# Kernel tuning notes

Measured on AMD Instinct MI355X. Metric: run time of the kernel, lower is better.

The kernel has to match this reference:

```python
import jax, jax.numpy as jnp
import numpy as np

B_, L_, D_ = 4, 4096, 256
EXPAND = 2
DI_ = EXPAND * D_      # 512 inner channels
H_ = 8                 # heads
P_ = DI_ // H_         # 64 head dim
N_ = 16                # d_state
K_ = 3                 # depthwise conv kernel


def setup_inputs() -> dict:
    key = jax.random.key(0)
    ks = jax.random.split(key, 32)

    def n(i, shape, s=0.02):
        return jax.random.normal(ks[i], shape, jnp.float32) * s

    inp = {"inputs": jax.random.normal(ks[0], (B_, L_, D_), jnp.float32)}
    i = 1
    for pre in ("f_", "b_"):
        inp[pre + "in_proj_w"] = n(i, (2 * DI_, D_)); i += 1
        inp[pre + "in_proj_b"] = jnp.zeros((2 * DI_,), jnp.float32)
        inp[pre + "x_proj_w"] = n(i, (DI_ + 2 * H_ * N_, DI_)); i += 1
        inp[pre + "x_proj_b"] = jnp.zeros((DI_ + 2 * H_ * N_,), jnp.float32)
        inp[pre + "dt_bias"] = jnp.full((DI_,), -4.0, jnp.float32)  # softplus -> small dt
        inp[pre + "A_log"] = jnp.log(jnp.tile(jnp.arange(1, N_ + 1, dtype=jnp.float32), (DI_, 1)))
        inp[pre + "D_skip"] = jnp.ones((DI_,), jnp.float32)
        inp[pre + "out_proj_w"] = n(i, (D_, DI_)); i += 1
        inp[pre + "out_proj_b"] = jnp.zeros((D_,), jnp.float32)
    inp["norm_w"] = jnp.ones((D_,), jnp.float32)
    inp["norm_b"] = jnp.zeros((D_,), jnp.float32)
    inp["conv_w"] = n(20, (D_, 1, K_), 0.1)   # depthwise: (out_ch, in_ch/groups=1, k)
    inp["conv_b"] = jnp.zeros((D_,), jnp.float32)
    return inp


def _layernorm(x, w, b):
    m = x.mean(-1, keepdims=True)
    v = ((x - m) ** 2).mean(-1, keepdims=True)
    return (x - m) * jax.lax.rsqrt(v + 1e-5) * w + b


def _mh_ssm(x, in_w, in_b, xp_w, xp_b, dt_b, A_log, D_skip, out_w, out_b):
    # Multihead selective-scan SSM (Mamba-style). x: (B, L, D)
    Bsz, L, _ = x.shape
    xz = x @ in_w.T + in_b                      # (B, L, 2*DI)
    xi, z = jnp.split(xz, 2, axis=-1)
    xi = jax.nn.silu(xi)                        # (B, L, DI)
    proj = xi @ xp_w.T + xp_b                   # (B, L, DI + 2*H*N)
    dt = jax.nn.softplus(proj[..., :DI_] + dt_b)        # (B, L, DI)
    Bm = proj[..., DI_:DI_ + H_ * N_].reshape(Bsz, L, H_, N_)
    Cm = proj[..., DI_ + H_ * N_:].reshape(Bsz, L, H_, N_)
    A = -jnp.exp(A_log).reshape(H_, P_, N_)     # (H, P, N), negative
    x4 = xi.reshape(Bsz, L, H_, P_)
    dt4 = dt.reshape(Bsz, L, H_, P_)

    def step(h, t):
        xt, dtt, Bt, Ct = t                     # (B,H,P), (B,H,P), (B,H,N), (B,H,N)
        dA = jnp.exp(dtt[..., None] * A)        # (B,H,P,N)
        h = h * dA + dtt[..., None] * Bt[:, :, None, :] * xt[..., None]
        y = jnp.einsum('bhpn,bhn->bhp', h, Ct)
        return h, y

    xs = (x4.transpose(1, 0, 2, 3), dt4.transpose(1, 0, 2, 3),
          Bm.transpose(1, 0, 2, 3), Cm.transpose(1, 0, 2, 3))
    h0 = jnp.zeros((Bsz, H_, P_, N_), x.dtype)
    _, ys = jax.lax.scan(step, h0, xs)          # ys: (L,B,H,P)
    y = ys.transpose(1, 0, 2, 3).reshape(Bsz, L, DI_) + xi * D_skip
    y = y * jax.nn.silu(z)                      # gating
    return y @ out_w.T + out_b                  # (B, L, D)


def reference(inputs,
              f_in_proj_w, f_in_proj_b, f_x_proj_w, f_x_proj_b, f_dt_bias,
              f_A_log, f_D_skip, f_out_proj_w, f_out_proj_b,
              b_in_proj_w, b_in_proj_b, b_x_proj_w, b_x_proj_b, b_dt_bias,
              b_A_log, b_D_skip, b_out_proj_w, b_out_proj_b,
              norm_w, norm_b, conv_w, conv_b):
    # Cascaded bidirectional SSM: backward(flip(norm(forward(x)))) then flip back
    y1 = _mh_ssm(inputs, f_in_proj_w, f_in_proj_b, f_x_proj_w, f_x_proj_b,
                 f_dt_bias, f_A_log, f_D_skip, f_out_proj_w, f_out_proj_b)
    y1n = jnp.flip(_layernorm(y1, norm_w, norm_b), axis=1)
    y2 = _mh_ssm(y1n, b_in_proj_w, b_in_proj_b, b_x_proj_w, b_x_proj_b,
                 b_dt_bias, b_A_log, b_D_skip, b_out_proj_w, b_out_proj_b)
    out = jnp.flip(y2, axis=1)
    # locality branch: depthwise Conv1d (groups=C) + exact GELU
    xt = inputs.transpose(0, 2, 1)              # (B, C, L)
    c = jax.lax.conv_general_dilated(
        xt, conv_w, window_strides=(1,), padding=[(1, 1)],
        dimension_numbers=('NCH', 'OIH', 'NCH'), feature_group_count=D_)
    c = jax.nn.gelu(c + conv_b[None, :, None], approximate=False)
    return out + c.transpose(0, 2, 1)
```

## Files before the change

### kernel.cpp

```cpp
#include <hip/hip_runtime.h>
#include <hip/hip_bf16.h>
#include <cstdint>
#include <cstddef>

#define B_  4
#define L_  4096
#define D_  256
#define DI_ 512
#define H_  8
#define P_  64
#define N_  16
#define M_  (B_ * L_)
#define PROJ_ (DI_ + 2 * H_ * N_)

#define NC_ 64
#define CL_ (L_ / NC_)
#define NSEQ_ (B_ * H_ * P_ * N_)
#define LOG2E_ 1.4426950408889634f

typedef __bf16 bf16x8 __attribute__((ext_vector_type(8)));
typedef __bf16 bf16x4 __attribute__((ext_vector_type(4)));
typedef float f32x4 __attribute__((ext_vector_type(4)));
typedef _Float16 f16x8 __attribute__((ext_vector_type(8)));

__device__ __forceinline__ void cp16_lds(const __hip_bfloat16* g, short* lds) {
    __builtin_amdgcn_global_load_lds(
        (const __attribute__((address_space(1))) void*)g,
        (__attribute__((address_space(3))) void*)lds, 16, 0, 0);
}

#define WS1 (2 * DI_ * D_)
#define WS2 (PROJ_ * DI_)
#define WS3 (D_ * DI_)
#define WC1 (WS1)
#define WC2 (WC1 + WS2)
#define WC3 (WC2 + WS3)
#define WC4 (WC3 + WS1)
#define WC5 (WC4 + WS2)
#define WC6 (WC5 + WS3)
#define WT8 (WC6 / 8)

__launch_bounds__(256)
__global__ void f2b_all(const float* __restrict__ i1,
                        const float* __restrict__ i2, const float* __restrict__ i3,
                        const float* __restrict__ i4, const float* __restrict__ i5,
                        const float* __restrict__ i6,
                        __hip_bfloat16* o1, __hip_bfloat16* o2,
                        __hip_bfloat16* o3, __hip_bfloat16* o4, __hip_bfloat16* o5,
                        __hip_bfloat16* o6) {
    for (int idx8 = blockIdx.x * 256 + threadIdx.x; idx8 < WT8;
         idx8 += gridDim.x * 256) {
        const int idx = idx8 * 8;
        const float* s; __hip_bfloat16* d; int off;
        if (idx < WC1)      { s = i1; d = o1; off = idx; }
        else if (idx < WC2) { s = i2; d = o2; off = idx - WC1; }
        else if (idx < WC3) { s = i3; d = o3; off = idx - WC2; }
        else if (idx < WC4) { s = i4; d = o4; off = idx - WC3; }
        else if (idx < WC5) { s = i5; d = o5; off = idx - WC4; }
        else                { s = i6; d = o6; off = idx - WC5; }
        const float4 f0 = *reinterpret_cast<const float4*>(s + off);
        const float4 f1 = *reinterpret_cast<const float4*>(s + off + 4);
        bf16x8 v;
        v[0] = (__bf16)f0.x; v[1] = (__bf16)f0.y;
        v[2] = (__bf16)f0.z; v[3] = (__bf16)f0.w;
        v[4] = (__bf16)f1.x; v[5] = (__bf16)f1.y;
        v[6] = (__bf16)f1.z; v[7] = (__bf16)f1.w;
        *reinterpret_cast<bf16x8*>(d + off) = v;
    }
}

template <int EPI, int AF32>
__launch_bounds__(256)
__global__ void gemm_mfma(const __hip_bfloat16* __restrict__ A,
                          const __hip_bfloat16* __restrict__ W,
                          const float* __restrict__ bias, int Kv,
                          __hip_bfloat16* __restrict__ zb,
                          __hip_bfloat16* __restrict__ obf,
                          const float* __restrict__ aux,
                          const float* __restrict__ A32) {
    __shared__ short As[128 * 64];
    __shared__ short Bs[128 * 64];
    const int tid = threadIdx.x;
    const int lane = tid & 63;
    const int wave = tid >> 6;
    const int bm = blockIdx.x * 128;
    const int bn = blockIdx.y * 128;
    const int wm = (wave >> 1) * 64;
    const int wn = (wave & 1) * 64;

    f32x4 acc[4][4];
#pragma unroll
    for (int i = 0; i < 4; ++i)
#pragma unroll
        for (int j = 0; j < 4; ++j) acc[i][j] = (f32x4)0.f;

    const int srow = lane >> 3;
    const int sx = lane & 7;
    const int ssegx = (sx ^ srow) * 8;
    const __hip_bfloat16* gA0 = A + (size_t)(bm + wave * 32 + srow) * Kv + ssegx;
    const __hip_bfloat16* gB0 = W + (size_t)(bn + wave * 32 + srow) * Kv + ssegx;
    short* lA0 = As + (wave * 32) * 64;
    short* lB0 = Bs + (wave * 32) * 64;

    const int fr = lane & 15;
    const int kq = lane >> 4;

    for (int k0 = 0; k0 < Kv; k0 += 64) {
        if (AF32) {
#pragma unroll
            for (int rb = 0; rb < 4; ++rb) {
                const int row = wave * 32 + rb * 8 + srow;
                const float* g = A32 + (size_t)(bm + row) * Kv + k0 + ssegx;
                const float4 f0 = *reinterpret_cast<const float4*>(g);
                const float4 f1 = *reinterpret_cast<const float4*>(g + 4);
                bf16x8 s;
                s[0] = (__bf16)f0.x; s[1] = (__bf16)f0.y;
                s[2] = (__bf16)f0.z; s[3] = (__bf16)f0.w;
                s[4] = (__bf16)f1.x; s[5] = (__bf16)f1.y;
                s[6] = (__bf16)f1.z; s[7] = (__bf16)f1.w;
                *reinterpret_cast<bf16x8*>(&As[row * 64 + sx * 8]) = s;
            }
        } else {
#pragma unroll
            for (int rb = 0; rb < 4; ++rb)
                cp16_lds(gA0 + (size_t)(rb * 8) * Kv + k0, lA0 + rb * 8 * 64);
        }
#pragma unroll
        for (int rb = 0; rb < 4; ++rb)
            cp16_lds(gB0 + (size_t)(rb * 8) * Kv + k0, lB0 + rb * 8 * 64);
        __syncthreads();
#pragma unroll
        for (int ks = 0; ks < 2; ++ks) {
            const int kgg = ks * 4 + kq;
            const int kslot = (kgg ^ (fr & 7)) * 8;
            bf16x8 af[4], bv[4];
#pragma unroll
            for (int i = 0; i < 4; ++i)
                af[i] = *reinterpret_cast<const bf16x8*>(
                    &As[(wm + i * 16 + fr) * 64 + kslot]);
#pragma unroll
            for (int j = 0; j < 4; ++j)
                bv[j] = *reinterpret_cast<const bf16x8*>(
                    &Bs[(wn + j * 16 + fr) * 64 + kslot]);
#pragma unroll
            for (int i = 0; i < 4; ++i)
#pragma unroll
                for (int j = 0; j < 4; ++j)
                    acc[i][j] = __builtin_amdgcn_mfma_f32_16x16x32_bf16(
                        af[i], bv[j], acc[i][j], 0, 0, 0);
        }
        __syncthreads();
    }

    const int n16 = lane & 15;
    const int r4 = (lane >> 4) * 4;
#pragma unroll
    for (int i = 0; i < 4; ++i) {
#pragma unroll
        for (int j = 0; j < 4; ++j) {
            const int cg = bn + wn + j * 16 + n16;
            const float bb = bias[cg];
#pragma unroll
            for (int v = 0; v < 4; ++v) {
                const int r = bm + wm + i * 16 + r4 + v;
                float val = acc[i][j][v] + bb;
                if (EPI == 1) {
                    if (cg < DI_) {
                        val = val / (1.f + __expf(-val));
                        obf[(size_t)r * DI_ + cg] = __float2bfloat16(val);
                    } else {
                        zb[(size_t)r * DI_ + cg - DI_] = __float2bfloat16(val);
                    }
                } else {
                    if (cg < DI_) {
                        const float x = val + aux[cg];
                        val = (x > 20.f) ? x : __logf(1.f + __expf(x));
                    }
                    obf[(size_t)r * PROJ_ + cg] = __float2bfloat16(val);
                }
            }
        }
    }
}

__launch_bounds__(256)
__global__ void gemm64_convout(const __hip_bfloat16* __restrict__ A,
                               const __hip_bfloat16* __restrict__ W,
                               const float* __restrict__ bias, int Kv,
                               float* __restrict__ out0,
                               const float* __restrict__ cw,
                               const float* __restrict__ cb,
                               const float* __restrict__ cinp) {
    __shared__ short As[64 * 64];
    __shared__ short Bs[64 * 64];
    const int tid = threadIdx.x;
    const int lane = tid & 63;
    const int wave = tid >> 6;
    const int bm = blockIdx.x * 64;
    const int bn = blockIdx.y * 64;
    const int wm = (wave >> 1) * 32;
    const int wn = (wave & 1) * 32;

    f32x4 acc[2][2];
#pragma unroll
    for (int i = 0; i < 2; ++i)
#pragma unroll
        for (int j = 0; j < 2; ++j) acc[i][j] = (f32x4)0.f;

    const int srow = lane >> 3;
    const int ssegx = ((lane & 7) ^ srow) * 8;
    const __hip_bfloat16* gA0 = A + (size_t)(bm + wave * 16 + srow) * Kv + ssegx;
    const __hip_bfloat16* gB0 = W + (size_t)(bn + wave * 16 + srow) * Kv + ssegx;
    short* lA0 = As + (wave * 16) * 64;
    short* lB0 = Bs + (wave * 16) * 64;

    const int fr = lane & 15;
    const int kq = lane >> 4;

    for (int k0 = 0; k0 < Kv; k0 += 64) {
#pragma unroll
        for (int rb = 0; rb < 2; ++rb) {
            cp16_lds(gA0 + (size_t)(rb * 8) * Kv + k0, lA0 + rb * 8 * 64);
            cp16_lds(gB0 + (size_t)(rb * 8) * Kv + k0, lB0 + rb * 8 * 64);
        }
        __syncthreads();
#pragma unroll
        for (int ks = 0; ks < 2; ++ks) {
            const int kgg = ks * 4 + kq;
            const int kslot = (kgg ^ (fr & 7)) * 8;
            bf16x8 af[2], bv[2];
#pragma unroll
            for (int i = 0; i < 2; ++i)
                af[i] = *reinterpret_cast<const bf16x8*>(
                    &As[(wm + i * 16 + fr) * 64 + kslot]);
#pragma unroll
            for (int j = 0; j < 2; ++j)
                bv[j] = *reinterpret_cast<const bf16x8*>(
                    &Bs[(wn + j * 16 + fr) * 64 + kslot]);
#pragma unroll
            for (int i = 0; i < 2; ++i)
#pragma unroll
                for (int j = 0; j < 2; ++j)
                    acc[i][j] = __builtin_amdgcn_mfma_f32_16x16x32_bf16(
                        af[i], bv[j], acc[i][j], 0, 0, 0);
        }
        __syncthreads();
    }

    const int n16 = lane & 15;
    const int r4 = (lane >> 4) * 4;
#pragma unroll
    for (int i = 0; i < 2; ++i) {
#pragma unroll
        for (int j = 0; j < 2; ++j) {
            const int cg = bn + wn + j * 16 + n16;
            const float bb = bias[cg];
#pragma unroll
            for (int v = 0; v < 4; ++v) {
                const int r = bm + wm + i * 16 + r4 + v;
                float val = acc[i][j][v] + bb;
                const int b = r >> 12;
                const int l = r & (L_ - 1);
                const int lo = L_ - 1 - l;
                const size_t base = ((size_t)(b << 12) + lo) * 256 + cg;
                float cv = fmaf(cinp[base], cw[cg * 3 + 1], cb[cg]);
                if (lo > 0) cv = fmaf(cinp[base - 256], cw[cg * 3 + 0], cv);
                if (lo + 1 < L_) cv = fmaf(cinp[base + 256], cw[cg * 3 + 2], cv);
                const float g = 0.5f * cv * (1.f + erff(cv * 0.70710678118654752f));
                out0[base] = val + g;
            }
        }
    }
}

__launch_bounds__(256)
__global__ void gemm_out_ln(const __hip_bfloat16* __restrict__ A,
                            const __hip_bfloat16* __restrict__ W,
                            const float* __restrict__ bias,
                            const float* __restrict__ lnw,
                            const float* __restrict__ lnb,
                            __hip_bfloat16* __restrict__ outb) {
    __shared__ short As[64 * 64];
    __shared__ short Ws[256 * 64];
    __shared__ float rs[2][4][64];
    const int tid = threadIdx.x;
    const int lane = tid & 63;
    const int wave = tid >> 6;
    const int bm = blockIdx.x * 64;
    const int Kv = DI_;

    f32x4 acc[4][4];
#pragma unroll
    for (int i = 0; i < 4; ++i)
#pragma unroll
        for (int j = 0; j < 4; ++j) acc[i][j] = (f32x4)0.f;

    const int srow = lane >> 3;
    const int ssegx = ((lane & 7) ^ srow) * 8;
    const __hip_bfloat16* gA0 = A + (size_t)(bm + wave * 16 + srow) * Kv + ssegx;
    const __hip_bfloat16* gW0 = W + (size_t)(wave * 64 + srow) * Kv + ssegx;
    short* lA0 = As + (wave * 16) * 64;
    short* lW0 = Ws + (wave * 64) * 64;

    const int fr = lane & 15;
    const int kq = lane >> 4;

    for (int k0 = 0; k0 < Kv; k0 += 64) {
#pragma unroll
        for (int rb = 0; rb < 2; ++rb)
            cp16_lds(gA0 + (size_t)(rb * 8) * Kv + k0, lA0 + rb * 8 * 64);
#pragma unroll
        for (int rb = 0; rb < 8; ++rb)
            cp16_lds(gW0 + (size_t)(rb * 8) * Kv + k0, lW0 + rb * 8 * 64);
        __syncthreads();
#pragma unroll
        for (int ks = 0; ks < 2; ++ks) {
            const int kgg = ks * 4 + kq;
            const int kslot = (kgg ^ (fr & 7)) * 8;
            bf16x8 af[4], bv[4];
#pragma unroll
            for (int i = 0; i < 4; ++i)
                af[i] = *reinterpret_cast<const bf16x8*>(
                    &As[(i * 16 + fr) * 64 + kslot]);
#pragma unroll
            for (int j = 0; j < 4; ++j)
                bv[j] = *reinterpret_cast<const bf16x8*>(
                    &Ws[(wave * 64 + j * 16 + fr) * 64 + kslot]);
#pragma unroll
            for (int i = 0; i < 4; ++i)
#pragma unroll
                for (int j = 0; j < 4; ++j)
                    acc[i][j] = __builtin_amdgcn_mfma_f32_16x16x32_bf16(
                        af[i], bv[j], acc[i][j], 0, 0, 0);
        }
        __syncthreads();
    }

    const int n16 = lane & 15;
    const int r4 = (lane >> 4) * 4;
#pragma unroll
    for (int j = 0; j < 4; ++j) {
        const float bb = bias[wave * 64 + j * 16 + n16];
#pragma unroll
        for (int i = 0; i < 4; ++i)
#pragma unroll
            for (int v = 0; v < 4; ++v) acc[i][j][v] += bb;
    }

#pragma unroll
    for (int i = 0; i < 4; ++i) {
#pragma unroll
        for (int v = 0; v < 4; ++v) {
            float s = 0.f, s2 = 0.f;
#pragma unroll
            for (int j = 0; j < 4; ++j) {
                const float t = acc[i][j][v];
                s += t; s2 = fmaf(t, t, s2);
            }
            s += __shfl_xor(s, 1); s2 += __shfl_xor(s2, 1);
            s += __shfl_xor(s, 2); s2 += __shfl_xor(s2, 2);
            s += __shfl_xor(s, 4); s2 += __shfl_xor(s2, 4);
            s += __shfl_xor(s, 8); s2 += __shfl_xor(s2, 8);
            if (n16 == 0) {
                rs[0][wave][i * 16 + r4 + v] = s;
                rs[1][wave][i * 16 + r4 + v] = s2;
            }
        }
    }
    __syncthreads();

#pragma unroll
    for (int i = 0; i < 4; ++i) {
#pragma unroll
        for (int v = 0; v < 4; ++v) {
            const int row = i * 16 + r4 + v;
            const float ts = rs[0][0][row] + rs[0][1][row] + rs[0][2][row] + rs[0][3][row];
            const float ts2 = rs[1][0][row] + rs[1][1][row] + rs[1][2][row] + rs[1][3][row];
            const float mean = ts * (1.f / 256.f);
            const float var = ts2 * (1.f / 256.f) - mean * mean;
            const float inv = rsqrtf(var + 1e-5f);
            const int rg = bm + row;
            const int b = rg >> 12;
            const int l = rg & (L_ - 1);
            const size_t drow = (size_t)((b << 12) + (L_ - 1 - l)) * 256;
#pragma unroll
            for (int j = 0; j < 4; ++j) {
                const int cg = wave * 64 + j * 16 + n16;
                const float o = (acc[i][j][v] - mean) * inv * lnw[cg] + lnb[cg];
                outb[drow + cg] = __float2bfloat16(o);
            }
        }
    }
}

__device__ __forceinline__ bool a_is_arith(const float* A2) {
    bool ok = true;
#pragma unroll
    for (int n = 1; n < N_; ++n)
        ok = ok && (fabsf(A2[n] - (float)(n + 1) * A2[0]) <= 1e-4f * fabsf(A2[n]));
    return ok;
}

__launch_bounds__(256)
__global__ void scan_chunk_state(const __hip_bfloat16* __restrict__ xi,
                                 const __hip_bfloat16* __restrict__ projb,
                                 const float* __restrict__ A_log,
                                 float* __restrict__ sS,
                                 _Float16* __restrict__ st_hend) {
    __shared__ float bsh[4][CL_][16];
    const int bh = blockIdx.x;
    const int b = bh >> 3;
    const int h = bh & 7;
    const int lane = threadIdx.x & 63;
    const int wave = threadIdx.x >> 6;
    const int chunk = blockIdx.y * 4 + wave;
    const int t0 = chunk * CL_;
    const int c = h * P_ + lane;
    const int bOff = DI_ + h * N_;

    {
#pragma unroll
        for (int r = 0; r < 4; ++r) {
            const int stp = r * 16 + (lane >> 2);
            const int j = (lane & 3) * 4;
            const bf16x4 v = *reinterpret_cast<const bf16x4*>(
                projb + ((size_t)b * L_ + t0 + stp) * PROJ_ + bOff + j);
            *reinterpret_cast<float4*>(&bsh[wave][stp][j]) =
                make_float4((float)v[0], (float)v[1], (float)v[2], (float)v[3]);
        }
    }

    float A2[N_], hs[N_];
#pragma unroll
    for (int n = 0; n < N_; ++n) {
        A2[n] = -__expf(A_log[c * N_ + n]) * LOG2E_;
        hs[n] = 0.f;
    }
    const bool fast = a_is_arith(A2);

    const __hip_bfloat16* pDt = projb + ((size_t)b * L_ + t0) * PROJ_ + c;
    const __hip_bfloat16* px = xi + ((size_t)b * L_ + t0) * DI_ + c;
    float S = 0.f;

    if (fast) {
        float dtb[2][4], xb[2][4];
#pragma unroll
        for (int i = 0; i < 4; ++i) {
            dtb[0][i] = __bfloat162float(pDt[(size_t)i * PROJ_]);
            xb[0][i] = __bfloat162float(px[(size_t)i * DI_]);
        }
#pragma unroll
        for (int k = 0; k < CL_ / 4; ++k) {
            const int cur = k & 1, nxt = cur ^ 1;
            if (k + 1 < CL_ / 4) {
#pragma unroll
                for (int i = 0; i < 4; ++i) {
                    dtb[nxt][i] = __bfloat162float(pDt[(size_t)((k + 1) * 4 + i) * PROJ_]);
                    xb[nxt][i] = __bfloat162float(px[(size_t)((k + 1) * 4 + i) * DI_]);
                }
            }
#pragma unroll
            for (int i = 0; i < 4; ++i) {
                const int t = k * 4 + i;
                const float dt_v = dtb[cur][i];
                const float dtx = dt_v * xb[cur][i];
                const float e1 = exp2f(dt_v * A2[0]);
                S += dt_v;
                const f32x4* bp = reinterpret_cast<const f32x4*>(&bsh[wave][t][0]);
                float dA = e1;
#pragma unroll
                for (int q = 0; q < 4; ++q) {
                    const f32x4 Bq = bp[q];
#pragma unroll
                    for (int j = 0; j < 4; ++j) {
                        hs[q * 4 + j] = fmaf(hs[q * 4 + j], dA, dtx * Bq[j]);
                        dA *= e1;
                    }
                }
            }
        }
    } else {
#pragma unroll 4
        for (int t = 0; t < CL_; ++t) {
            const float dt_v = __bfloat162float(pDt[(size_t)t * PROJ_]);
            const float xv = __bfloat162float(px[(size_t)t * DI_]);
            const float dtx = dt_v * xv;
            S += dt_v;
#pragma unroll
            for (int n = 0; n < N_; ++n) {
                const float dA = exp2f(dt_v * A2[n]);
                hs[n] = fmaf(hs[n], dA, dtx * bsh[wave][t][n]);
            }
        }
    }

    sS[(size_t)chunk * (B_ * DI_) + (size_t)(bh * P_ + lane)] = S;
    const size_t s0 = (size_t)chunk * NSEQ_ + ((size_t)(bh * P_ + lane)) * N_;
    f16x8 h0, h1;
#pragma unroll
    for (int j = 0; j < 8; ++j) { h0[j] = (_Float16)hs[j]; h1[j] = (_Float16)hs[8 + j]; }
    *reinterpret_cast<f16x8*>(st_hend + s0) = h0;
    *reinterpret_cast<f16x8*>(st_hend + s0 + 8) = h1;
}

__launch_bounds__(128)
__global__ void scan_combine(const float* __restrict__ sS,
                             const float* __restrict__ A_log,
                             _Float16* __restrict__ st_prod,
                             const _Float16* __restrict__ st_hend) {
    const int gtid = blockIdx.x * 128 + threadIdx.x;
    const int s = gtid >> 1;
    const int u = gtid & 1;
    const int lane = threadIdx.x & 63;
    const int seqc = s >> 4;
    const int n = s & 15;
    const int cA = seqc & (DI_ - 1);
    const float A2n = -__expf(A_log[cA * N_ + n]) * LOG2E_;

    float Hloc[32], Dr[32];
    float H = 0.f, D = 1.f;
#pragma unroll
    for (int kk = 0; kk < 32; ++kk) {
        const int k = u * 32 + kk;
        const size_t o = (size_t)k * NSEQ_ + s;
        const float Pv = exp2f(A2n * sS[(size_t)k * (B_ * DI_) + seqc]);
        const float Ev = (float)st_hend[o];
        Hloc[kk] = H; Dr[kk] = D;
        H = fmaf(Pv, H, Ev);
        D *= Pv;
    }
    const float Hmid = __shfl(H, lane & ~1);
    if (u == 0) {
#pragma unroll
        for (int kk = 0; kk < 32; ++kk) {
            const size_t o = (size_t)kk * NSEQ_ + s;
            st_prod[o] = (_Float16)Hloc[kk];
        }
    } else {
#pragma unroll
        for (int kk = 0; kk < 32; ++kk) {
            const size_t o = (size_t)(32 + kk) * NSEQ_ + s;
            st_prod[o] = (_Float16)fmaf(Dr[kk], Hmid, Hloc[kk]);
        }
    }
}

__launch_bounds__(256)
__global__ void scan_chunk_out(const __hip_bfloat16* __restrict__ xi,
                               const __hip_bfloat16* __restrict__ z,
                               const __hip_bfloat16* __restrict__ projb,
                               const float* __restrict__ A_log,
                               const float* __restrict__ D_skip,
                               const _Float16* __restrict__ st_hin,
                               __hip_bfloat16* __restrict__ yg) {
    __shared__ float bc[4][CL_][32];
    const int bh = blockIdx.x;
    const int b = bh >> 3;
    const int h = bh & 7;
    const int lane = threadIdx.x & 63;
    const int wave = threadIdx.x >> 6;
    const int chunk = blockIdx.y * 4 + wave;
    const int t0 = chunk * CL_;
    const int c = h * P_ + lane;
    const int bOff = DI_ + h * N_;
    const int cOff = DI_ + H_ * N_ + h * N_;

    {
#pragma unroll
        for (int r = 0; r < 8; ++r) {
            const int stp = r * 8 + (lane >> 3);
            const int j = (lane & 7) * 4;
            const int soff = (j < 16) ? (bOff + j) : (cOff + (j - 16));
            const bf16x4 v = *reinterpret_cast<const bf16x4*>(
                projb + ((size_t)b * L_ + t0 + stp) * PROJ_ + soff);
            *reinterpret_cast<float4*>(&bc[wave][stp][j]) =
                make_float4((float)v[0], (float)v[1], (float)v[2], (float)v[3]);
        }
    }

    float A2[N_], hs[N_];
    const size_t s0 = (size_t)chunk * NSEQ_ + ((size_t)(bh * P_ + lane)) * N_;
    {
        const f16x8 a0 = *reinterpret_cast<const f16x8*>(st_hin + s0);
        const f16x8 a1 = *reinterpret_cast<const f16x8*>(st_hin + s0 + 8);
#pragma unroll
        for (int j = 0; j < 8; ++j) { hs[j] = (float)a0[j]; hs[8 + j] = (float)a1[j]; }
    }
#pragma unroll
    for (int n = 0; n < N_; ++n)
        A2[n] = -__expf(A_log[c * N_ + n]) * LOG2E_;
    const bool fast = a_is_arith(A2);
    const float Dv = D_skip[c];

    const __hip_bfloat16* pDt = projb + ((size_t)b * L_ + t0) * PROJ_ + c;
    const __hip_bfloat16* px = xi + ((size_t)b * L_ + t0) * DI_ + c;
    const __hip_bfloat16* pz = z + ((size_t)b * L_ + t0) * DI_ + c;
    __hip_bfloat16* py = yg + ((size_t)b * L_ + t0) * DI_ + c;

    if (fast) {
        float dtb[2][4], xb[2][4], zb[2][4];
#pragma unroll
        for (int i = 0; i < 4; ++i) {
            dtb[0][i] = __bfloat162float(pDt[(size_t)i * PROJ_]);
            xb[0][i] = __bfloat162float(px[(size_t)i * DI_]);
            zb[0][i] = __bfloat162float(pz[(size_t)i * DI_]);
        }
#pragma unroll
        for (int k = 0; k < CL_ / 4; ++k) {
            const int cur = k & 1, nxt = cur ^ 1;
            if (k + 1 < CL_ / 4) {
#pragma unroll
                for (int i = 0; i < 4; ++i) {
                    const int t = (k + 1) * 4 + i;
                    dtb[nxt][i] = __bfloat162float(pDt[(size_t)t * PROJ_]);
                    xb[nxt][i] = __bfloat162float(px[(size_t)t * DI_]);
                    zb[nxt][i] = __bfloat162float(pz[(size_t)t * DI_]);
                }
            }
#pragma unroll
            for (int i = 0; i < 4; ++i) {
                const int t = k * 4 + i;
                const float dt_v = dtb[cur][i];
                const float xv = xb[cur][i];
                const float zv = zb[cur][i];
                const float dtx = dt_v * xv;
                const float e1 = exp2f(dt_v * A2[0]);
                const f32x4* bp = reinterpret_cast<const f32x4*>(&bc[wave][t][0]);
                float dA = e1;
                float y = 0.f;
#pragma unroll
                for (int q = 0; q < 4; ++q) {
                    const f32x4 Bq = bp[q];
                    const f32x4 Cq = bp[4 + q];
#pragma unroll
                    for (int j = 0; j < 4; ++j) {
                        hs[q * 4 + j] = fmaf(hs[q * 4 + j], dA, dtx * Bq[j]);
                        y = fmaf(hs[q * 4 + j], Cq[j], y);
                        dA *= e1;
                    }
                }
                const float g = zv / (1.f + __expf(-zv));
                py[(size_t)t * DI_] = __float2bfloat16((y + Dv * xv) * g);
            }
        }
    } else {
#pragma unroll 4
        for (int t = 0; t < CL_; ++t) {
            const float dt_v = __bfloat162float(pDt[(size_t)t * PROJ_]);
            const float xv = __bfloat162float(px[(size_t)t * DI_]);
            const float zv = __bfloat162float(pz[(size_t)t * DI_]);
            const float dtx = dt_v * xv;
            float y = 0.f;
#pragma unroll
            for (int n = 0; n < N_; ++n) {
                const float dA = exp2f(dt_v * A2[n]);
                hs[n] = fmaf(hs[n], dA, dtx * bc[wave][t][n]);
                y = fmaf(hs[n], bc[wave][t][16 + n], y);
            }
            const float g = zv / (1.f + __expf(-zv));
            py[(size_t)t * DI_] = __float2bfloat16((y + Dv * xv) * g);
        }
    }
}

extern "C" void kernel_launch(void* const* d_in, const int* in_sizes, int n_in,
                              void* d_out, int out_size, void* d_ws, size_t ws_size,
                              hipStream_t stream) {
    const float* inputs = (const float*)d_in[0];
    const float* f_in_w = (const float*)d_in[1];
    const float* f_in_b = (const float*)d_in[2];
    const float* f_xp_w = (const float*)d_in[3];
    const float* f_xp_b = (const float*)d_in[4];
    const float* f_dt_b = (const float*)d_in[5];
    const float* f_A = (const float*)d_in[6];
    const float* f_D = (const float*)d_in[7];
    const float* f_out_w = (const float*)d_in[8];
    const float* f_out_b = (const float*)d_in[9];
    const float* b_in_w = (const float*)d_in[10];
    const float* b_in_b = (const float*)d_in[11];
    const float* b_xp_w = (const float*)d_in[12];
    const float* b_xp_b = (const float*)d_in[13];
    const float* b_dt_b = (const float*)d_in[14];
    const float* b_A = (const float*)d_in[15];
    const float* b_D = (const float*)d_in[16];
    const float* b_out_w = (const float*)d_in[17];
    const float* b_out_b = (const float*)d_in[18];
    const float* norm_w = (const float*)d_in[19];
    const float* norm_b = (const float*)d_in[20];
    const float* conv_w = (const float*)d_in[21];
    const float* conv_b = (const float*)d_in[22];
    float* out = (float*)d_out;

    float* ws = (float*)d_ws;
    _Float16* st_prod = (_Float16*)ws;
    float* slot1 = ws + (size_t)NSEQ_ * 128;
    _Float16* st_hend = (_Float16*)slot1;
    float* zslot   = slot1 + (size_t)NSEQ_ * 128;
    __hip_bfloat16* z_bf = (__hip_bfloat16*)zslot;
    float* pslot   = zslot + (size_t)M_ * DI_;
    __hip_bfloat16* proj_bf = (__hip_bfloat16*)pslot;
    float* y1      = pslot + (size_t)M_ * PROJ_;
    float* sS      = y1;
    __hip_bfloat16* xi_bf = (__hip_bfloat16*)(y1 + (size_t)M_ * D_);
    __hip_bfloat16* yg_bf = xi_bf + (size_t)M_ * DI_;
    __hip_bfloat16* a_bf  = yg_bf + (size_t)M_ * DI_;
    __hip_bfloat16* wpool = a_bf + (size_t)M_ * D_;
    __hip_bfloat16* f_in_wb  = wpool;
    __hip_bfloat16* f_xp_wb  = f_in_wb + 2 * DI_ * D_;
    __hip_bfloat16* f_out_wb = f_xp_wb + PROJ_ * DI_;
    __hip_bfloat16* b_in_wb  = f_out_wb + D_ * DI_;
    __hip_bfloat16* b_xp_wb  = b_in_wb + 2 * DI_ * D_;
    __hip_bfloat16* b_out_wb = b_xp_wb + PROJ_ * DI_;

    const dim3 blk(256);
    const dim3 g_in(M_ / 128, (2 * DI_) / 128);
    const dim3 g_xp(M_ / 128, PROJ_ / 128);
    const dim3 g_out64(M_ / 64, D_ / 64);
    const dim3 g_oln(M_ / 64);
    const dim3 g_chunk(B_ * H_, NC_ / 4);
    const dim3 g_comb(NSEQ_ * 2 / 128);
    const dim3 blk_comb(128);

    f2b_all<<<dim3(768), blk, 0, stream>>>(f_in_w, f_xp_w, f_out_w,
                                           b_in_w, b_xp_w, b_out_w,
                                           f_in_wb, f_xp_wb, f_out_wb,
                                           b_in_wb, b_xp_wb, b_out_wb);

    gemm_mfma<1, 1><<<g_in, blk, 0, stream>>>(nullptr, f_in_wb, f_in_b, D_,
                                              z_bf, xi_bf, nullptr, inputs);
    gemm_mfma<2, 0><<<g_xp, blk, 0, stream>>>(xi_bf, f_xp_wb, f_xp_b, DI_,
                                              nullptr, proj_bf, f_dt_b, nullptr);
    scan_chunk_state<<<g_chunk, blk, 0, stream>>>(xi_bf, proj_bf, f_A,
                                                  sS, st_hend);
    scan_combine<<<g_comb, blk_comb, 0, stream>>>(sS, f_A, st_prod, st_hend);
    scan_chunk_out<<<g_chunk, blk, 0, stream>>>(xi_bf, z_bf, proj_bf, f_A, f_D,
                                                st_prod, yg_bf);
    gemm_out_ln<<<g_oln, blk, 0, stream>>>(yg_bf, f_out_wb, f_out_b,
                                           norm_w, norm_b, a_bf);

    gemm_mfma<1, 0><<<g_in, blk, 0, stream>>>(a_bf, b_in_wb, b_in_b, D_,
                                              z_bf, xi_bf, nullptr, nullptr);
    gemm_mfma<2, 0><<<g_xp, blk, 0, stream>>>(xi_bf, b_xp_wb, b_xp_b, DI_,
                                              nullptr, proj_bf, b_dt_b, nullptr);
    scan_chunk_state<<<g_chunk, blk, 0, stream>>>(xi_bf, proj_bf, b_A,
                                                  sS, st_hend);
    scan_combine<<<g_comb, blk_comb, 0, stream>>>(sS, b_A, st_prod, st_hend);
    scan_chunk_out<<<g_chunk, blk, 0, stream>>>(xi_bf, z_bf, proj_bf, b_A, b_D,
                                                st_prod, yg_bf);
    gemm64_convout<<<g_out64, blk, 0, stream>>>(yg_bf, b_out_wb, b_out_b, DI_,
                                                out, conv_w, conv_b, inputs);
}
```

Measured before the change: 358.4 us.

## Double scan chunk count and rework combine into four-way LDS prefix

```diff
diff --git a/kernel.cpp b/kernel.cpp
--- a/kernel.cpp
+++ b/kernel.cpp
@@ -13,7 +13,7 @@
 #define M_  (B_ * L_)
 #define PROJ_ (DI_ + 2 * H_ * N_)
 
-#define NC_ 64
+#define NC_ 128
 #define CL_ (L_ / NC_)
 #define NSEQ_ (B_ * H_ * P_ * N_)
 #define LOG2E_ 1.4426950408889634f
@@ -420,7 +420,7 @@
 
     {
 #pragma unroll
-        for (int r = 0; r < 4; ++r) {
+        for (int r = 0; r < CL_ / 16; ++r) {
             const int stp = r * 16 + (lane >> 2);
             const int j = (lane & 3) * 4;
             const bf16x4 v = *reinterpret_cast<const bf16x4*>(
@@ -508,10 +508,10 @@
                              const float* __restrict__ A_log,
                              _Float16* __restrict__ st_prod,
                              const _Float16* __restrict__ st_hend) {
-    const int gtid = blockIdx.x * 128 + threadIdx.x;
-    const int s = gtid >> 1;
-    const int u = gtid & 1;
-    const int lane = threadIdx.x & 63;
+    __shared__ float sH[128], sD[128];
+    const int sl = threadIdx.x & 31;
+    const int u = threadIdx.x >> 5;
+    const int s = blockIdx.x * 32 + sl;
     const int seqc = s >> 4;
     const int n = s & 15;
     const int cA = seqc & (DI_ - 1);
@@ -529,19 +529,17 @@
         H = fmaf(Pv, H, Ev);
         D *= Pv;
     }
-    const float Hmid = __shfl(H, lane & ~1);
-    if (u == 0) {
-#pragma unroll
-        for (int kk = 0; kk < 32; ++kk) {
-            const size_t o = (size_t)kk * NSEQ_ + s;
-            st_prod[o] = (_Float16)Hloc[kk];
-        }
-    } else {
-#pragma unroll
-        for (int kk = 0; kk < 32; ++kk) {
-            const size_t o = (size_t)(32 + kk) * NSEQ_ + s;
-            st_prod[o] = (_Float16)fmaf(Dr[kk], Hmid, Hloc[kk]);
-        }
+    sH[threadIdx.x] = H; sD[threadIdx.x] = D;
+    __syncthreads();
+    float Hs = 0.f;
+#pragma unroll
+    for (int v = 0; v < 3; ++v) {
+        if (u > v) Hs = fmaf(sD[v * 32 + sl], Hs, sH[v * 32 + sl]);
+    }
+#pragma unroll
+    for (int kk = 0; kk < 32; ++kk) {
+        const size_t o = (size_t)(u * 32 + kk) * NSEQ_ + s;
+        st_prod[o] = (_Float16)fmaf(Dr[kk], Hs, Hloc[kk]);
     }
 }
 
@@ -567,7 +565,7 @@
 
     {
 #pragma unroll
-        for (int r = 0; r < 8; ++r) {
+        for (int r = 0; r < CL_ / 8; ++r) {
             const int stp = r * 8 + (lane >> 3);
             const int j = (lane & 7) * 4;
             const int soff = (j < 16) ? (bOff + j) : (cOff + (j - 16));
@@ -718,7 +716,7 @@
     const dim3 g_out64(M_ / 64, D_ / 64);
     const dim3 g_oln(M_ / 64);
     const dim3 g_chunk(B_ * H_, NC_ / 4);
-    const dim3 g_comb(NSEQ_ * 2 / 128);
+    const dim3 g_comb(NSEQ_ / 32);
     const dim3 blk_comb(128);
 
     f2b_all<<<dim3(768), blk, 0, stream>>>(f_in_w, f_xp_w, f_out_w,
```

Result: no change. 359.1 us (+0.2%).
